# Performance work log

Measured on AMD Instinct MI355X. Metric: run time of the kernel, lower is better.

Reference implementation:

```python
import jax, jax.numpy as jnp
import numpy as np

N_NODES = 100000
N_EDGES = 1600000
D_IN = 64
D_OUT = 64


def setup_inputs() -> dict:
    key = jax.random.key(0)
    k1, k2, k3, k4, k5 = jax.random.split(key, 5)
    x = jax.random.normal(k1, (N_NODES, D_IN), dtype=jnp.float32)
    edge_index = jax.random.randint(k2, (2, N_EDGES), 0, N_NODES, dtype=jnp.int64)
    dist_vec = jax.random.uniform(k3, (N_EDGES,), dtype=jnp.float32)
    # Linear params (xavier-uniform-like scale for W)
    limit = float(np.sqrt(6.0 / (D_IN + D_OUT)))
    W = jax.random.uniform(k4, (D_OUT, D_IN), minval=-limit, maxval=limit, dtype=jnp.float32)
    b = jax.random.uniform(k5, (D_OUT,), minval=-limit, maxval=limit, dtype=jnp.float32)
    return {"x": x, "edge_index": edge_index, "dist_vec": dist_vec, "W": W, "b": b}


def reference(x, edge_index, dist_vec, W, b):
    row, col = edge_index[0], edge_index[1]
    n = x.shape[0]
    # degree of destination (col) nodes
    deg = jax.ops.segment_sum(jnp.ones_like(dist_vec), col, num_segments=n)
    deg_inv_sqrt = jnp.where(deg > 0, jax.lax.rsqrt(deg), 0.0)
    norm = deg_inv_sqrt[row] * deg_inv_sqrt[col]  # [E]
    w = jnp.exp(-dist_vec ** 2) * norm            # [E]
    # sparse.mm(adj, x): out[row] += w * x[col]
    msgs = w[:, None] * x[col]                    # [E, D_IN]
    side_embed = jax.ops.segment_sum(msgs, row, num_segments=n)  # [N, D_IN]
    return side_embed @ W.T + b
```

## Files before the change

kernel.cpp:

```cpp
#include <hip/hip_runtime.h>
#include <hip/hip_fp16.h>


constexpr int NN   = 100000;
constexpr int NE   = 1600000;
constexpr int D    = 64;
constexpr int NRB  = (NN + 127) / 128;
constexpr int NCB  = (NN + 255) / 256;
constexpr int HB   = 256;
constexpr int HT   = 1024;
constexpr int CHUNK = NE / HB;
constexpr int NSR  = NRB * HB;
constexpr int NSCC = NCB * HB;
constexpr int NST  = NSR + NSCC;
constexpr int SCB  = 1024;
constexpr int SCG  = (NST + SCB - 1) / SCB;
constexpr int CAP  = 3072;

using f16x8 = __attribute__((ext_vector_type(8))) _Float16;
using f32x4 = __attribute__((ext_vector_type(4))) float;

__global__ void __launch_bounds__(HT)
hist2_kernel(const int* __restrict__ row, const int* __restrict__ col,
             int* __restrict__ hist) {
    __shared__ int hr[NRB], hc[NCB];
    const int t = threadIdx.x;
    for (int i = t; i < NRB; i += HT) hr[i] = 0;
    for (int i = t; i < NCB; i += HT) hc[i] = 0;
    __syncthreads();
    const int e0 = blockIdx.x * CHUNK;
    for (int e = e0 + t; e < e0 + CHUNK; e += HT) {
        atomicAdd(&hr[row[e] >> 7], 1);
        atomicAdd(&hc[col[e] >> 8], 1);
    }
    __syncthreads();
    for (int i = t; i < NRB; i += HT) hist[i * HB + blockIdx.x] = hr[i];
    for (int i = t; i < NCB; i += HT) hist[NSR + i * HB + blockIdx.x] = hc[i];
}

__global__ void scanpart_kernel(const int* __restrict__ a, int* __restrict__ bsum) {
    __shared__ int red[16];
    const int t = threadIdx.x;
    const int i = blockIdx.x * SCB + t;
    int s = (i < NST) ? a[i] : 0;
    #pragma unroll
    for (int o = 1; o < 64; o <<= 1) s += __shfl_xor(s, o);
    if ((t & 63) == 0) red[t >> 6] = s;
    __syncthreads();
    if (t < 16) {
        int ss = red[t];
        #pragma unroll
        for (int o = 1; o < 16; o <<= 1) ss += __shfl_xor(ss, o);
        if (t == 0) bsum[blockIdx.x] = ss;
    }
}

__global__ void scanblk_kernel(const int* __restrict__ bsum, int* __restrict__ boff) {
    __shared__ int wsum[8], wsum2[8];
    const int t = threadIdx.x;
    const int lane = t & 63;
    const int w = t >> 6;
    const int v = (t < SCG) ? bsum[t] : 0;
    int s = v;
    #pragma unroll
    for (int o = 1; o < 64; o <<= 1) { int u = __shfl_up(s, o); if (lane >= o) s += u; }
    if (lane == 63) wsum[w] = s;
    __syncthreads();
    if (t < 8) {
        int ss = wsum[t];
        #pragma unroll
        for (int o = 1; o < 8; o <<= 1) { int u = __shfl_up(ss, o); if (t >= o) ss += u; }
        wsum2[t] = ss;
    }
    __syncthreads();
    const int excl = (w ? wsum2[w - 1] : 0) + (s - v);
    if (t < SCG) boff[t] = excl;
}

__global__ void scanfinal_kernel(int* __restrict__ a, const int* __restrict__ boff) {
    __shared__ int wsum[16], wsum2[16];
    const int t = threadIdx.x;
    const int i = blockIdx.x * SCB + t;
    const int lane = t & 63;
    const int w = t >> 6;
    const int v = (i < NST) ? a[i] : 0;
    int s = v;
    #pragma unroll
    for (int o = 1; o < 64; o <<= 1) { int u = __shfl_up(s, o); if (lane >= o) s += u; }
    if (lane == 63) wsum[w] = s;
    __syncthreads();
    if (t < 16) {
        int ss = wsum[t];
        #pragma unroll
        for (int o = 1; o < 16; o <<= 1) { int u = __shfl_up(ss, o); if (t >= o) ss += u; }
        wsum2[t] = ss;
    }
    __syncthreads();
    const int excl = boff[blockIdx.x] + (w ? wsum2[w - 1] : 0) + (s - v);
    if (i < NST) a[i] = excl;
}

__global__ void __launch_bounds__(HT)
scatcol_kernel(const int* __restrict__ col, const int* __restrict__ hoff,
               unsigned char* __restrict__ colidx) {
    __shared__ int cur[NCB];
    const int t = threadIdx.x;
    for (int i = t; i < NCB; i += HT) cur[i] = hoff[NSR + i * HB + blockIdx.x] - NE;
    __syncthreads();
    const int e0 = blockIdx.x * CHUNK;
    for (int e = e0 + t; e < e0 + CHUNK; e += HT) {
        const int c = col[e];
        const int pos = atomicAdd(&cur[c >> 8], 1);
        colidx[pos] = (unsigned char)(c & 255);
    }
}

__global__ void __launch_bounds__(256)
coldinv_kernel(const int* __restrict__ hoff, const unsigned char* __restrict__ colidx,
               float* __restrict__ dinv) {
    __shared__ int cnt[256];
    const int t = threadIdx.x;
    const int b = blockIdx.x;
    cnt[t] = 0;
    __syncthreads();
    const int s0 = hoff[NSR + b * HB] - NE;
    const int s1 = (b + 1 < NCB) ? (hoff[NSR + (b + 1) * HB] - NE) : NE;
    for (int k = s0 + t; k < s1; k += 256) atomicAdd(&cnt[colidx[k]], 1);
    __syncthreads();
    const int n = b * 256 + t;
    if (n < NN) {
        const int d = cnt[t];
        dinv[n] = (d > 0) ? rsqrtf((float)d) : 0.0f;
    }
}

__global__ void __launch_bounds__(HT)
scatter1_kernel(const int* __restrict__ row, const int* __restrict__ col,
                const float* __restrict__ dist, const float* __restrict__ dinv,
                const int* __restrict__ hoff, int2* __restrict__ edges8) {
    __shared__ int cur[NRB];
    const int t = threadIdx.x;
    for (int i = t; i < NRB; i += HT) cur[i] = hoff[i * HB + blockIdx.x];
    __syncthreads();
    const int e0 = blockIdx.x * CHUNK;
    for (int e = e0 + t; e < e0 + CHUNK; e += HT) {
        const int r = row[e];
        const int c = col[e];
        const float dv = dist[e];
        const float wv = expf(-dv * dv) * dinv[c];
        const unsigned w15 = (unsigned)(wv * 32767.0f + 0.5f);
        const int pos = atomicAdd(&cur[r >> 7], 1);
        edges8[pos] = make_int2((int)((w15 << 17) | (unsigned)c), r);
    }
}

__global__ void __launch_bounds__(256)
sort2_kernel(const int* __restrict__ hoff, const int2* __restrict__ edges8,
             unsigned* __restrict__ edges4, int* __restrict__ rowstart) {
    __shared__ int2 raw8[CAP];
    __shared__ int cnt[128], cur[128], wtot[2];
    const int t = threadIdx.x;
    const int b = blockIdx.x;
    const int lane = t & 63;
    if (t < 128) cnt[t] = 0;
    const int s0 = hoff[b * HB];
    const int s1 = (b + 1 < NRB) ? hoff[(b + 1) * HB] : NE;
    int ne = s1 - s0;
    ne = (ne < CAP) ? ne : CAP;
    for (int k = t; k < ne; k += 256) raw8[k] = edges8[s0 + k];
    __syncthreads();
    for (int k = t; k < ne; k += 256) atomicAdd(&cnt[raw8[k].y & 127], 1);
    __syncthreads();
    int s = 0, v = 0;
    if (t < 128) {
        v = cnt[t];
        s = v;
        #pragma unroll
        for (int o = 1; o < 64; o <<= 1) { int u = __shfl_up(s, o); if (lane >= o) s += u; }
        if (lane == 63) wtot[t >> 6] = s;
    }
    __syncthreads();
    if (t < 128) {
        const int excl = (s - v) + ((t >= 64) ? wtot[0] : 0);
        cur[t] = excl;
        rowstart[b * 128 + t] = s0 + excl;
    }
    __syncthreads();
    for (int k = t; k < ne; k += 256) {
        const int pos = atomicAdd(&cur[raw8[k].y & 127], 1);
        edges4[s0 + pos] = (unsigned)raw8[k].x;
    }
}

__global__ void __launch_bounds__(256)
ygemm_kernel(const float* __restrict__ x, const float* __restrict__ W,
             __half* __restrict__ y) {
    const int t = threadIdx.x;
    const int m  = t & 15;
    const int kb = (t & 63) >> 4;
    f16x8 bf[4][2];
    #pragma unroll
    for (int jt = 0; jt < 4; ++jt) {
        #pragma unroll
        for (int kh = 0; kh < 2; ++kh) {
            const float* wp = W + (size_t)(jt * 16 + m) * 64 + kh * 32 + kb * 8;
            const float4 w0 = *reinterpret_cast<const float4*>(wp);
            const float4 w1 = *reinterpret_cast<const float4*>(wp + 4);
            f16x8 f;
            f[0] = (_Float16)w0.x; f[1] = (_Float16)w0.y;
            f[2] = (_Float16)w0.z; f[3] = (_Float16)w0.w;
            f[4] = (_Float16)w1.x; f[5] = (_Float16)w1.y;
            f[6] = (_Float16)w1.z; f[7] = (_Float16)w1.w;
            bf[jt][kh] = f;
        }
    }
    const int wid = (blockIdx.x * 256 + t) >> 6;
    const int nw  = (gridDim.x * 256) >> 6;
    for (int nt = wid; nt < NN / 16; nt += nw) {
        const int n0 = nt * 16;
        f16x8 af[2];
        #pragma unroll
        for (int kh = 0; kh < 2; ++kh) {
            const float* xp = x + (size_t)(n0 + m) * 64 + kh * 32 + kb * 8;
            const float4 x0 = *reinterpret_cast<const float4*>(xp);
            const float4 x1 = *reinterpret_cast<const float4*>(xp + 4);
            f16x8 f;
            f[0] = (_Float16)x0.x; f[1] = (_Float16)x0.y;
            f[2] = (_Float16)x0.z; f[3] = (_Float16)x0.w;
            f[4] = (_Float16)x1.x; f[5] = (_Float16)x1.y;
            f[6] = (_Float16)x1.z; f[7] = (_Float16)x1.w;
            af[kh] = f;
        }
        #pragma unroll
        for (int jt = 0; jt < 4; ++jt) {
            f32x4 acc = {0.f, 0.f, 0.f, 0.f};
            acc = __builtin_amdgcn_mfma_f32_16x16x32_f16(af[0], bf[jt][0], acc, 0, 0, 0);
            acc = __builtin_amdgcn_mfma_f32_16x16x32_f16(af[1], bf[jt][1], acc, 0, 0, 0);
            #pragma unroll
            for (int r = 0; r < 4; ++r) {
                y[(size_t)(n0 + kb * 4 + r) * 64 + jt * 16 + m] = __float2half(acc[r]);
            }
        }
    }
}

__global__ void __launch_bounds__(256)
gather_kernel(const int* __restrict__ rowstart, const unsigned* __restrict__ edges4,
              const float* __restrict__ dinvg, const __half* __restrict__ y,
              const float* __restrict__ bias, float* __restrict__ out) {
    const int t = threadIdx.x;
    const int lane = t & 63;
    const int wv = t >> 6;
    const int sub = lane >> 3;
    const int ch8 = (lane & 7) << 3;
    constexpr float WSCL = 1.0f / 32767.0f;
    const float4 b0 = *reinterpret_cast<const float4*>(bias + ch8);
    const float4 b1 = *reinterpret_cast<const float4*>(bias + ch8 + 4);

    const int nwaves = gridDim.x * 4;
    for (int n = blockIdx.x * 4 + wv; n < NN; n += nwaves) {
        const int s0 = rowstart[n];
        const int s1 = rowstart[n + 1];
        float a0 = 0.f, a1 = 0.f, a2 = 0.f, a3 = 0.f;
        float a4 = 0.f, a5 = 0.f, a6 = 0.f, a7 = 0.f;
        for (int p0 = s0; p0 < s1; p0 += 8) {
            const int pp = p0 + sub;
            const int ppc = (pp < s1) ? pp : (s1 - 1);
            const unsigned m = edges4[ppc];
            const int c = (int)(m & 0x1FFFFu);
            float wgt = (float)(m >> 17) * WSCL;
            wgt = (pp < s1) ? wgt : 0.0f;
            const float4 raw = *reinterpret_cast<const float4*>(y + (size_t)c * 64 + ch8);
            const __half2* h2 = reinterpret_cast<const __half2*>(&raw);
            const float2 f0 = __half22float2(h2[0]);
            const float2 f1 = __half22float2(h2[1]);
            const float2 f2 = __half22float2(h2[2]);
            const float2 f3 = __half22float2(h2[3]);
            a0 += wgt * f0.x; a1 += wgt * f0.y; a2 += wgt * f1.x; a3 += wgt * f1.y;
            a4 += wgt * f2.x; a5 += wgt * f2.y; a6 += wgt * f3.x; a7 += wgt * f3.y;
        }
        #pragma unroll
        for (int o = 8; o < 64; o <<= 1) {
            a0 += __shfl_xor(a0, o); a1 += __shfl_xor(a1, o);
            a2 += __shfl_xor(a2, o); a3 += __shfl_xor(a3, o);
            a4 += __shfl_xor(a4, o); a5 += __shfl_xor(a5, o);
            a6 += __shfl_xor(a6, o); a7 += __shfl_xor(a7, o);
        }
        if (sub == 0) {
            const float dn = dinvg[n];
            const float4 o0 = make_float4(b0.x + dn * a0, b0.y + dn * a1,
                                          b0.z + dn * a2, b0.w + dn * a3);
            const float4 o1 = make_float4(b1.x + dn * a4, b1.y + dn * a5,
                                          b1.z + dn * a6, b1.w + dn * a7);
            float* op = out + (size_t)n * 64 + ch8;
            *reinterpret_cast<float4*>(op)     = o0;
            *reinterpret_cast<float4*>(op + 4) = o1;
        }
    }
}

extern "C" void kernel_launch(void* const* d_in, const int* in_sizes, int n_in,
                              void* d_out, int out_size, void* d_ws, size_t ws_size,
                              hipStream_t stream) {
    const float* x    = (const float*)d_in[0];
    const int*   ei   = (const int*)d_in[1];
    const float* dist = (const float*)d_in[2];
    const float* W    = (const float*)d_in[3];
    const float* b    = (const float*)d_in[4];
    float* out = (float*)d_out;

    const int* row = ei;
    const int* col = ei + NE;

    int2*     edges8   = (int2*)d_ws;
    __half*   y        = (__half*)d_ws;
    unsigned* edges4   = (unsigned*)(edges8 + NE);
    int*      hist     = (int*)(edges4 + NE);
    int*      rowstart = hist + NST;
    float*    dinv     = (float*)(rowstart + NRB * 128 + 1);
    int*      bsum     = (int*)(dinv + NN);
    int*      boff     = bsum + SCG;
    unsigned char* colidx = (unsigned char*)(boff + SCG);

    hist2_kernel    <<<HB, HT, 0, stream>>>(row, col, hist);
    scanpart_kernel <<<SCG, SCB, 0, stream>>>(hist, bsum);
    scanblk_kernel  <<<1, 512, 0, stream>>>(bsum, boff);
    scanfinal_kernel<<<SCG, SCB, 0, stream>>>(hist, boff);
    scatcol_kernel  <<<HB, HT, 0, stream>>>(col, hist, colidx);
    coldinv_kernel  <<<NCB, 256, 0, stream>>>(hist, colidx, dinv);
    scatter1_kernel <<<HB, HT, 0, stream>>>(row, col, dist, dinv, hist, edges8);
    sort2_kernel    <<<NRB, 256, 0, stream>>>(hist, edges8, edges4, rowstart);
    ygemm_kernel    <<<1024, 256, 0, stream>>>(x, W, y);
    gather_kernel   <<<4096, 256, 0, stream>>>(rowstart, edges4, dinv, y, b, out);
}
```

Measured before the change: 125.4 us.

## Fuse row/col scatters and merge per-bucket sort into gather kernel

Row and column bucket scatters are merged into one pass. Each edge payload now packs the local row (7 bits), an 8-bit exp weight and the column index into 32 bits, which removes the 8-byte intermediate edge array. The per-128-row bucket sort now runs in shared memory inside the gather kernel, and the col-side dinv factor is fetched per edge at gather time. This cuts two kernel launches and one global round trip of the edge list. In exchange the weight is quantised to 8 bits (a precision loss), each edge needs an extra dinv gather, and the gather grid shrinks to one block per 128 rows.

```diff
diff --git a/kernel.cpp b/kernel.cpp
--- a/kernel.cpp
+++ b/kernel.cpp
@@ -101,94 +101,45 @@
 }
 
 __global__ void __launch_bounds__(HT)
-scatcol_kernel(const int* __restrict__ col, const int* __restrict__ hoff,
-               unsigned char* __restrict__ colidx) {
-    __shared__ int cur[NCB];
-    const int t = threadIdx.x;
-    for (int i = t; i < NCB; i += HT) cur[i] = hoff[NSR + i * HB + blockIdx.x] - NE;
-    __syncthreads();
-    const int e0 = blockIdx.x * CHUNK;
-    for (int e = e0 + t; e < e0 + CHUNK; e += HT) {
-        const int c = col[e];
-        const int pos = atomicAdd(&cur[c >> 8], 1);
-        colidx[pos] = (unsigned char)(c & 255);
-    }
-}
-
-__global__ void __launch_bounds__(256)
-coldinv_kernel(const int* __restrict__ hoff, const unsigned char* __restrict__ colidx,
-               float* __restrict__ dinv) {
-    __shared__ int cnt[256];
-    const int t = threadIdx.x;
-    const int b = blockIdx.x;
-    cnt[t] = 0;
-    __syncthreads();
-    const int s0 = hoff[NSR + b * HB] - NE;
-    const int s1 = (b + 1 < NCB) ? (hoff[NSR + (b + 1) * HB] - NE) : NE;
-    for (int k = s0 + t; k < s1; k += 256) atomicAdd(&cnt[colidx[k]], 1);
-    __syncthreads();
-    const int n = b * 256 + t;
-    if (n < NN) {
-        const int d = cnt[t];
-        dinv[n] = (d > 0) ? rsqrtf((float)d) : 0.0f;
-    }
-}
-
-__global__ void __launch_bounds__(HT)
-scatter1_kernel(const int* __restrict__ row, const int* __restrict__ col,
-                const float* __restrict__ dist, const float* __restrict__ dinv,
-                const int* __restrict__ hoff, int2* __restrict__ edges8) {
-    __shared__ int cur[NRB];
-    const int t = threadIdx.x;
-    for (int i = t; i < NRB; i += HT) cur[i] = hoff[i * HB + blockIdx.x];
+scatboth_kernel(const int* __restrict__ row, const int* __restrict__ col,
+                const float* __restrict__ dist, const int* __restrict__ hoff,
+                unsigned* __restrict__ payload, unsigned char* __restrict__ colidx) {
+    __shared__ int cur_r[NRB];
+    __shared__ int cur_c[NCB];
+    const int t = threadIdx.x;
+    for (int i = t; i < NRB; i += HT) cur_r[i] = hoff[i * HB + blockIdx.x];
+    for (int i = t; i < NCB; i += HT) cur_c[i] = hoff[NSR + i * HB + blockIdx.x] - NE;
     __syncthreads();
     const int e0 = blockIdx.x * CHUNK;
     for (int e = e0 + t; e < e0 + CHUNK; e += HT) {
         const int r = row[e];
         const int c = col[e];
         const float dv = dist[e];
-        const float wv = expf(-dv * dv) * dinv[c];
-        const unsigned w15 = (unsigned)(wv * 32767.0f + 0.5f);
-        const int pos = atomicAdd(&cur[r >> 7], 1);
-        edges8[pos] = make_int2((int)((w15 << 17) | (unsigned)c), r);
+        const float wv = expf(-dv * dv);
+        const unsigned w8 = (unsigned)(wv * 255.0f + 0.5f);
+        const int pr = atomicAdd(&cur_r[r >> 7], 1);
+        payload[pr] = ((unsigned)(r & 127) << 25) | (w8 << 17) | (unsigned)c;
+        const int pc = atomicAdd(&cur_c[c >> 8], 1);
+        colidx[pc] = (unsigned char)(c & 255);
     }
 }
 
 __global__ void __launch_bounds__(256)
-sort2_kernel(const int* __restrict__ hoff, const int2* __restrict__ edges8,
-             unsigned* __restrict__ edges4, int* __restrict__ rowstart) {
-    __shared__ int2 raw8[CAP];
-    __shared__ int cnt[128], cur[128], wtot[2];
+coldinv_kernel(const int* __restrict__ hoff, const unsigned char* __restrict__ colidx,
+               float* __restrict__ dinv) {
+    __shared__ int cnt[256];
     const int t = threadIdx.x;
     const int b = blockIdx.x;
-    const int lane = t & 63;
-    if (t < 128) cnt[t] = 0;
-    const int s0 = hoff[b * HB];
-    const int s1 = (b + 1 < NRB) ? hoff[(b + 1) * HB] : NE;
-    int ne = s1 - s0;
-    ne = (ne < CAP) ? ne : CAP;
-    for (int k = t; k < ne; k += 256) raw8[k] = edges8[s0 + k];
-    __syncthreads();
-    for (int k = t; k < ne; k += 256) atomicAdd(&cnt[raw8[k].y & 127], 1);
-    __syncthreads();
-    int s = 0, v = 0;
-    if (t < 128) {
-        v = cnt[t];
-        s = v;
-        #pragma unroll
-        for (int o = 1; o < 64; o <<= 1) { int u = __shfl_up(s, o); if (lane >= o) s += u; }
-        if (lane == 63) wtot[t >> 6] = s;
-    }
-    __syncthreads();
-    if (t < 128) {
-        const int excl = (s - v) + ((t >= 64) ? wtot[0] : 0);
-        cur[t] = excl;
-        rowstart[b * 128 + t] = s0 + excl;
-    }
-    __syncthreads();
-    for (int k = t; k < ne; k += 256) {
-        const int pos = atomicAdd(&cur[raw8[k].y & 127], 1);
-        edges4[s0 + pos] = (unsigned)raw8[k].x;
+    cnt[t] = 0;
+    __syncthreads();
+    const int s0 = hoff[NSR + b * HB] - NE;
+    const int s1 = (b + 1 < NCB) ? (hoff[NSR + (b + 1) * HB] - NE) : NE;
+    for (int k = s0 + t; k < s1; k += 256) atomicAdd(&cnt[colidx[k]], 1);
+    __syncthreads();
+    const int n = b * 256 + t;
+    if (n < NN) {
+        const int d = cnt[t];
+        dinv[n] = (d > 0) ? rsqrtf((float)d) : 0.0f;
     }
 }
 
@@ -244,32 +195,77 @@
     }
 }
 
-__global__ void __launch_bounds__(256)
-gather_kernel(const int* __restrict__ rowstart, const unsigned* __restrict__ edges4,
-              const float* __restrict__ dinvg, const __half* __restrict__ y,
-              const float* __restrict__ bias, float* __restrict__ out) {
+__global__ void __launch_bounds__(512)
+gather_fused_kernel(const int* __restrict__ hoff, const unsigned* __restrict__ payload,
+                    const float* __restrict__ dinvg, const __half* __restrict__ y,
+                    const float* __restrict__ bias, float* __restrict__ out) {
+    __shared__ unsigned stage[CAP];
+    __shared__ unsigned sorted[CAP];
+    __shared__ int cnt[128], cur[128], rs[129], wtot[2];
+    __shared__ float dinv_s[128];
     const int t = threadIdx.x;
     const int lane = t & 63;
     const int wv = t >> 6;
+    const int b = blockIdx.x;
     const int sub = lane >> 3;
     const int ch8 = (lane & 7) << 3;
-    constexpr float WSCL = 1.0f / 32767.0f;
+    constexpr float WSCL = 1.0f / 255.0f;
     const float4 b0 = *reinterpret_cast<const float4*>(bias + ch8);
     const float4 b1 = *reinterpret_cast<const float4*>(bias + ch8 + 4);
 
-    const int nwaves = gridDim.x * 4;
-    for (int n = blockIdx.x * 4 + wv; n < NN; n += nwaves) {
-        const int s0 = rowstart[n];
-        const int s1 = rowstart[n + 1];
+    if (t < 128) {
+        cnt[t] = 0;
+        const int n = b * 128 + t;
+        dinv_s[t] = (n < NN) ? dinvg[n] : 0.0f;
+    }
+    const int s0g = hoff[b * HB];
+    const int s1g = (b + 1 < NRB) ? hoff[(b + 1) * HB] : NE;
+    int ne = s1g - s0g;
+    ne = (ne < CAP) ? ne : CAP;
+    __syncthreads();
+    for (int k = t; k < ne; k += 512) {
+        const unsigned p = payload[s0g + k];
+        stage[k] = p;
+        atomicAdd(&cnt[p >> 25], 1);
+    }
+    __syncthreads();
+    int s = 0, v = 0;
+    if (t < 128) {
+        v = cnt[t];
+        s = v;
+        #pragma unroll
+        for (int o = 1; o < 64; o <<= 1) { int u = __shfl_up(s, o); if (lane >= o) s += u; }
+        if (lane == 63) wtot[t >> 6] = s;
+    }
+    __syncthreads();
+    if (t < 128) {
+        const int excl = (s - v) + ((t >= 64) ? wtot[0] : 0);
+        cur[t] = excl;
+        rs[t] = excl;
+        if (t == 0) rs[128] = wtot[0] + wtot[1];
+    }
+    __syncthreads();
+    for (int k = t; k < ne; k += 512) {
+        const unsigned p = stage[k];
+        const int pos = atomicAdd(&cur[p >> 25], 1);
+        sorted[pos] = p;
+    }
+    __syncthreads();
+
+    for (int ln = wv; ln < 128; ln += 8) {
+        const int n = b * 128 + ln;
+        if (n >= NN) break;
+        const int e0 = rs[ln];
+        const int e1 = rs[ln + 1];
         float a0 = 0.f, a1 = 0.f, a2 = 0.f, a3 = 0.f;
         float a4 = 0.f, a5 = 0.f, a6 = 0.f, a7 = 0.f;
-        for (int p0 = s0; p0 < s1; p0 += 8) {
+        for (int p0 = e0; p0 < e1; p0 += 8) {
             const int pp = p0 + sub;
-            const int ppc = (pp < s1) ? pp : (s1 - 1);
-            const unsigned m = edges4[ppc];
+            const int ppc = (pp < e1) ? pp : (e1 - 1);
+            const unsigned m = sorted[ppc];
             const int c = (int)(m & 0x1FFFFu);
-            float wgt = (float)(m >> 17) * WSCL;
-            wgt = (pp < s1) ? wgt : 0.0f;
+            float wgt = (float)((m >> 17) & 255u) * WSCL * dinvg[c];
+            wgt = (pp < e1) ? wgt : 0.0f;
             const float4 raw = *reinterpret_cast<const float4*>(y + (size_t)c * 64 + ch8);
             const __half2* h2 = reinterpret_cast<const __half2*>(&raw);
             const float2 f0 = __half22float2(h2[0]);
@@ -287,7 +283,7 @@
             a6 += __shfl_xor(a6, o); a7 += __shfl_xor(a7, o);
         }
         if (sub == 0) {
-            const float dn = dinvg[n];
+            const float dn = dinv_s[ln];
             const float4 o0 = make_float4(b0.x + dn * a0, b0.y + dn * a1,
                                           b0.z + dn * a2, b0.w + dn * a3);
             const float4 o1 = make_float4(b1.x + dn * a4, b1.y + dn * a5,
@@ -312,24 +308,20 @@
     const int* row = ei;
     const int* col = ei + NE;
 
-    int2*     edges8   = (int2*)d_ws;
-    __half*   y        = (__half*)d_ws;
-    unsigned* edges4   = (unsigned*)(edges8 + NE);
-    int*      hist     = (int*)(edges4 + NE);
-    int*      rowstart = hist + NST;
-    float*    dinv     = (float*)(rowstart + NRB * 128 + 1);
-    int*      bsum     = (int*)(dinv + NN);
-    int*      boff     = bsum + SCG;
+    unsigned* payload = (unsigned*)d_ws;
+    __half*   y       = (__half*)(payload + NE);
+    int*      hist    = (int*)(y + (size_t)NN * 64);
+    float*    dinv    = (float*)(hist + NST);
+    int*      bsum    = (int*)(dinv + NN);
+    int*      boff    = bsum + SCG;
     unsigned char* colidx = (unsigned char*)(boff + SCG);
 
+    ygemm_kernel    <<<1024, 256, 0, stream>>>(x, W, y);
     hist2_kernel    <<<HB, HT, 0, stream>>>(row, col, hist);
     scanpart_kernel <<<SCG, SCB, 0, stream>>>(hist, bsum);
     scanblk_kernel  <<<1, 512, 0, stream>>>(bsum, boff);
     scanfinal_kernel<<<SCG, SCB, 0, stream>>>(hist, boff);
-    scatcol_kernel  <<<HB, HT, 0, stream>>>(col, hist, colidx);
+    scatboth_kernel <<<HB, HT, 0, stream>>>(row, col, dist, hist, payload, colidx);
     coldinv_kernel  <<<NCB, 256, 0, stream>>>(hist, colidx, dinv);
-    scatter1_kernel <<<HB, HT, 0, stream>>>(row, col, dist, dinv, hist, edges8);
-    sort2_kernel    <<<NRB, 256, 0, stream>>>(hist, edges8, edges4, rowstart);
-    ygemm_kernel    <<<1024, 256, 0, stream>>>(x, W, y);
-    gather_kernel   <<<4096, 256, 0, stream>>>(rowstart, edges4, dinv, y, b, out);
-}
+    gather_fused_kernel<<<NRB, 512, 0, stream>>>(hist, payload, dinv, y, b, out);
+}
```

After: 120.5 us. 1.04x faster.
